# Kernel optimization log

Hardware: AMD Instinct MI355X
Metric: run time of the kernel (lower is better)

The kernel has to match this reference:

```python
import jax, jax.numpy as jnp
import numpy as np
from jax import lax

B, IC, OC, H, W_DIM, K = 8, 64, 64, 256, 512, 3
BLUR_1D = [1.0, 3.0, 3.0, 1.0]
FACTOR = 2
GAIN = 1.0


def _blur_kernel():
    # setup_resample_kernel: outer product of 1D kernel, normalized to sum 1
    k = np.asarray(BLUR_1D, dtype=np.float32)
    k = np.outer(k, k)
    k = k / np.sum(k)
    return k  # [4,4]


def setup_inputs() -> dict:
    key = jax.random.key(0)
    ks = jax.random.split(key, 5)
    x = jax.random.normal(ks[0], (B, IC, H, H), dtype=jnp.float32)
    w = jax.random.normal(ks[1], (B, W_DIM), dtype=jnp.float32)
    # init_std = 1.0 for both weights since lrmul = 1.0
    w_conv = jax.random.normal(ks[2], (K, K, IC, OC), dtype=jnp.float32)
    w_dense = jax.random.normal(ks[3], (W_DIM, IC), dtype=jnp.float32)
    b_mod = jnp.zeros((IC,), dtype=jnp.float32)
    return {"x": x, "w": w, "w_conv": w_conv, "w_dense": w_dense, "b_mod": b_mod}


def reference(x, w, w_conv, w_dense, b_mod):
    k = w_conv.shape[0]
    ic, oc = w_conv.shape[2], w_conv.shape[3]

    # runtime coefs (equalized lr): he_std = gain / sqrt(fan_in), lrmul = 1
    coef_conv = 1.0 / np.sqrt(k * k * ic)
    coef_dense = 1.0 / np.sqrt(w.shape[1])

    # style = Dense(w) + bias (linear act, gain 1) + 1.0   -> [B, IC]
    style = w @ (coef_dense * w_dense) + b_mod + 1.0

    # modulate: [B,k,k,IC,OC]
    wmod = (coef_conv * w_conv)[None] * style[:, None, None, :, None]
    # demodulate over (kh, kw, ic)
    d = lax.rsqrt(jnp.sum(jnp.square(wmod), axis=(1, 2, 3)) + 1e-8)  # [B,OC]
    wmod = wmod * d[:, None, None, None, :]

    # per-sample grouped transposed conv (upsample x2) == lhs-dilated cross-corr
    # with the unflipped modulated weight, padding k-1 on each side.
    w_oihw = jnp.transpose(wmod, (0, 4, 3, 1, 2))  # [B,OC,IC,k,k]

    def up_conv(xb, wb):
        return lax.conv_general_dilated(
            xb[None], wb, window_strides=(1, 1),
            padding=[(k - 1, k - 1), (k - 1, k - 1)],
            lhs_dilation=(FACTOR, FACTOR),
            dimension_numbers=("NCHW", "OIHW", "NCHW"))[0]

    y = jax.vmap(up_conv)(x, w_oihw)  # [B,OC,(H-1)*2+k,(W-1)*2+k] = [B,OC,513,513]

    # upfirdn blur: kernel scaled by gain * factor**2, pad0 = pad1 = 1,
    # true convolution (kernel flipped in reference) applied depthwise.
    kb = jnp.asarray(_blur_kernel() * (GAIN * FACTOR ** 2))  # [4,4]
    fw = kb[::-1, ::-1][None, None]  # [1,1,4,4]
    b_, c_, s1, s2 = y.shape
    y = lax.conv_general_dilated(
        y.reshape(b_ * c_, 1, s1, s2), fw, window_strides=(1, 1),
        padding=[(1, 1), (1, 1)],
        dimension_numbers=("NCHW", "OIHW", "NCHW"))
    # output spatial: s1 + 2 - 4 + 1 = 2H
    return y.reshape(b_, c_, y.shape[2], y.shape[3])
```

## Files before the change

kernel.cpp:

```cpp
#include <hip/hip_runtime.h>

#define NB 8
#define IC 64
#define OC 64
#define HH 256
#define WD 512
#define PP 258

typedef __bf16 bf16x8 __attribute__((ext_vector_type(8)));
typedef float f32x16 __attribute__((ext_vector_type(16)));

__device__ inline void compute_E(const float* __restrict__ w_conv, float stv,
                                 int oc, float E[6][6]) {
  const float coef_conv = 1.0f / 24.0f;
  const float s = stv * coef_conv;
  const int ic = threadIdx.x & 63;

  float wm[3][3];
  float ssq = 0.f;
  #pragma unroll
  for (int kh = 0; kh < 3; ++kh)
    #pragma unroll
    for (int kw = 0; kw < 3; ++kw) {
      float v = w_conv[((kh * 3 + kw) * IC + ic) * OC + oc] * s;
      wm[kh][kw] = v;
      ssq += v * v;
    }
  #pragma unroll
  for (int off = 32; off > 0; off >>= 1) ssq += __shfl_xor(ssq, off);
  const float d = rsqrtf(ssq + 1e-8f);
  #pragma unroll
  for (int kh = 0; kh < 3; ++kh)
    #pragma unroll
    for (int kw = 0; kw < 3; ++kw) wm[kh][kw] *= d;

  const float g[4] = {0.25f, 0.75f, 0.75f, 0.25f};
  #pragma unroll
  for (int a = 0; a < 6; ++a)
    #pragma unroll
    for (int c = 0; c < 6; ++c) {
      float acc = 0.f;
      #pragma unroll
      for (int dh = 0; dh < 3; ++dh) {
        int u = a - dh;
        if (u < 0 || u > 3) continue;
        #pragma unroll
        for (int dw = 0; dw < 3; ++dw) {
          int v = c - dw;
          if (v < 0 || v > 3) continue;
          acc = fmaf(wm[dh][dw], g[u] * g[v], acc);
        }
      }
      E[a][c] = acc;
    }
}

__device__ inline float style_of(const float* __restrict__ w,
                                 const float* __restrict__ w_dense,
                                 const float* __restrict__ b_mod, int b,
                                 int ic) {
  const float coef_dense = 0.044194173824159216f;
  const float* wr = w + b * WD;
  float acc = 0.f;
  for (int k = 0; k < WD; ++k) acc = fmaf(wr[k], w_dense[k * IC + ic], acc);
  return acc * coef_dense + b_mod[ic] + 1.0f;
}

__global__ __launch_bounds__(64) void pwfs_kernel(
    const float* __restrict__ w, const float* __restrict__ w_dense,
    const float* __restrict__ b_mod, const float* __restrict__ w_conv,
    __bf16* __restrict__ PWf) {
  const int oc = blockIdx.x;
  const int b = blockIdx.y;
  const int ic = threadIdx.x;

  float stv = style_of(w, w_dense, b_mod, b, ic);
  float E[6][6];
  compute_E(w_conv, stv, oc, E);

  const int ks = ic >> 4;
  const int h = (ic >> 3) & 1;
  const int e = ic & 7;
  const int lane = (oc & 31) + 32 * h;
  const int ocg = oc >> 5;

  #pragma unroll
  for (int pp = 0; pp < 2; ++pp)
    #pragma unroll
    for (int pq = 0; pq < 2; ++pq) {
      const int ph = pp * 2 + pq;
      #pragma unroll
      for (int j = 0; j < 3; ++j)
        #pragma unroll
        for (int l = 0; l < 3; ++l) {
          const int tap = j * 3 + l;
          float val = E[2 * j + 1 - pp][2 * l + 1 - pq];
          size_t off =
              ((size_t)(((((b * 4 + ph) * 9 + tap) * 2 + ocg) * 4 + ks)) * 64 +
               lane) * 8 + e;
          PWf[off] = (__bf16)val;
        }
    }
}

#define XS 268
__global__ __launch_bounds__(256) void xtp_kernel(const float* __restrict__ x,
                                                  __bf16* __restrict__ xTg) {
  __shared__ unsigned short buf[64 * XS];
  const int tid = threadIdx.x;
  const int m = blockIdx.x;
  const int b = blockIdx.y;

  if (m == 256) {
    uint4 z = make_uint4(0, 0, 0, 0);
    for (int i = tid; i < 8224; i += 256) {
      int pix = i >> 3;
      int sub = i & 7;
      int pr, pc;
      if (pix < 258) {
        pr = 0; pc = pix;
      } else if (pix < 516) {
        pr = 257; pc = pix - 258;
      } else {
        int rem = pix - 516;
        pr = 1 + (rem >> 1);
        pc = (rem & 1) ? 257 : 0;
      }
      *(uint4*)(xTg + ((size_t)(b * PP + pr) * PP + pc) * 64 + sub * 8) = z;
    }
    return;
  }

  const int ln = tid & 63, grp = tid >> 6;
  #pragma unroll
  for (int p = 0; p < 16; ++p) {
    const int ic = p * 4 + grp;
    float4 v = *(const float4*)(x + ((size_t)(b * 64 + ic) * 256 + m) * 256 +
                                ln * 4);
    ushort4 u4;
    u4.x = __builtin_bit_cast(unsigned short, (__bf16)v.x);
    u4.y = __builtin_bit_cast(unsigned short, (__bf16)v.y);
    u4.z = __builtin_bit_cast(unsigned short, (__bf16)v.z);
    u4.w = __builtin_bit_cast(unsigned short, (__bf16)v.w);
    *(ushort4*)&buf[ic * XS + ln * 4] = u4;
  }
  __syncthreads();
  #pragma unroll
  for (int it = 0; it < 8; ++it) {
    int pix = it * 32 + (tid >> 3);
    int g = tid & 7;
    bf16x8 o;
    #pragma unroll
    for (int e = 0; e < 8; ++e)
      o[e] = __builtin_bit_cast(__bf16, buf[(g * 8 + e) * XS + pix]);
    *(bf16x8*)(xTg + ((size_t)(b * PP + m + 1) * PP + (pix + 1)) * 64 +
               g * 8) = o;
  }
}

#define CMT 4
#define XR 6
#define XC 34

#define GLD_LDS(src, dst)                                                \
  __builtin_amdgcn_global_load_lds(                                      \
      (const __attribute__((address_space(1))) void*)(src),              \
      (__attribute__((address_space(3))) void*)(dst), 16, 0, 0)

__device__ __forceinline__ void stage6(const __bf16* __restrict__ xTg, int b,
                                       int m0, int n0, __bf16* xsbuf, int wv,
                                       int lane) {
  if (wv < XR) {
    const int row = wv;
    const size_t srow = (size_t)(b * PP + m0 + row) * PP;
    __bf16* ldsrow = xsbuf + row * (XC * 64);
    #pragma unroll
    for (int q = 0; q < 4; ++q) {
      int pix = q * 8 + (lane >> 3);
      int g = (lane & 7) ^ (pix & 7);
      const __bf16* src = xTg + (srow + (n0 + pix)) * 64 + g * 8;
      GLD_LDS(src, ldsrow + q * 512);
    }
    if (lane < 16) {
      int pix = 32 + (lane >> 3);
      int g = (lane & 7) ^ (pix & 7);
      const __bf16* src = xTg + (srow + (n0 + pix)) * 64 + g * 8;
      GLD_LDS(src, ldsrow + 2048);
    }
  }
}

__global__ __launch_bounds__(512, 2) void conv32a_kernel(
    const __bf16* __restrict__ xTg, const __bf16* __restrict__ PWf,
    float* __restrict__ out) {
  __shared__ __bf16 xs[2][XR * XC * 64];

  const int tid = threadIdx.x;
  const int lane = tid & 63;
  const int wv = tid >> 6;
  const int pq = wv & 1;
  const int pp = (wv >> 1) & 1;
  const int og = wv >> 2;

  const int raw = blockIdx.x;
  const int bid = (raw & 7) * 64 + (raw >> 3);
  const int mtile = bid & 63;
  const int b = bid >> 6;
  const int m0 = mtile * CMT;

  const int ln31 = lane & 31;
  const int lh = lane >> 5;
  const int ph = b * 4 + pp * 2 + pq;
  const bf16x8* Awave =
      (const bf16x8*)PWf + ((size_t)ph * 72 + og * 4) * 64 + lane;

  bf16x8 A[9][4];
  #pragma unroll
  for (int tap = 0; tap < 9; ++tap)
    #pragma unroll
    for (int ks = 0; ks < 4; ++ks) A[tap][ks] = Awave[(tap * 8 + ks) * 64];

  stage6(xTg, b, m0, 0, &xs[0][0], wv, lane);
  asm volatile("s_waitcnt vmcnt(0)" ::: "memory");
  __builtin_amdgcn_s_barrier();

  #pragma unroll 1
  for (int t = 0; t < 8; ++t) {
    const int n0 = t * 32;
    if (t < 7) stage6(xTg, b, m0, n0 + 32, &xs[(t + 1) & 1][0], wv, lane);

    const __bf16* xb = &xs[t & 1][0];

    f32x16 acc[4];
    #pragma unroll
    for (int mw = 0; mw < 4; ++mw)
      #pragma unroll
      for (int e = 0; e < 16; ++e) acc[mw][e] = 0.f;

    #pragma unroll
    for (int ks = 0; ks < 4; ++ks) {
      #pragma unroll
      for (int l = 0; l < 3; ++l) {
        bf16x8 Bf[6];
        const int col_t = ln31 + l;
        const int gneed = ks * 2 + lh;
        #pragma unroll
        for (int r = 0; r < 6; ++r) {
          Bf[r] = *(const bf16x8*)(xb + ((r * XC + col_t) * 8 +
                                         (gneed ^ (col_t & 7))) * 8);
        }
        __builtin_amdgcn_s_setprio(1);
        #pragma unroll
        for (int r = 0; r < 6; ++r) {
          #pragma unroll
          for (int j = 0; j < 3; ++j) {
            const int mw = r - j;
            if (mw >= 0 && mw < 4) {
              acc[mw] = __builtin_amdgcn_mfma_f32_32x32x16_bf16(
                  A[j * 3 + l][ks], Bf[r], acc[mw], 0, 0, 0);
            }
          }
        }
        __builtin_amdgcn_s_setprio(0);
      }
    }

    #pragma unroll
    for (int mw = 0; mw < 4; ++mw) {
      const int p = 2 * (m0 + mw) + pp;
      #pragma unroll
      for (int rr = 0; rr < 16; ++rr) {
        const int oc_loc = (rr & 3) + 8 * (rr >> 2) + 4 * lh;
        const int oc = og * 32 + oc_loc;
        size_t off =
            ((size_t)(b * 64 + oc) * 512 + p) * 512 + 2 * (n0 + ln31) + pq;
        out[off] = acc[mw][rr];
      }
    }

    if (t < 7) {
      asm volatile("s_waitcnt vmcnt(63)" ::: "memory");
      __builtin_amdgcn_s_barrier();
    }
  }
}

__global__ __launch_bounds__(64) void pw_kernel(
    const float* __restrict__ w, const float* __restrict__ w_dense,
    const float* __restrict__ b_mod, const float* __restrict__ w_conv,
    float* __restrict__ PW) {
  const int oc = blockIdx.x;
  const int b = blockIdx.y;
  const int ic = threadIdx.x;
  float stv = style_of(w, w_dense, b_mod, b, ic);
  float E[6][6];
  compute_E(w_conv, stv, oc, E);
  #pragma unroll
  for (int pp = 0; pp < 2; ++pp)
    #pragma unroll
    for (int pq = 0; pq < 2; ++pq)
      #pragma unroll
      for (int j = 0; j < 3; ++j)
        #pragma unroll
        for (int l = 0; l < 3; ++l)
          PW[(((size_t)((b * 4 + pp * 2 + pq) * OC + oc) * IC + ic) * 9) +
             j * 3 + l] = E[2 * j + 1 - pp][2 * l + 1 - pq];
}

#define MT 16
#define NT 64
#define ICC 8
#define XROWS 18
#define XCOLS 66
#define XSTRIDE 68

__global__ __launch_bounds__(256) void conv_kernel(
    const float* __restrict__ x, const float* __restrict__ PW,
    float* __restrict__ out) {
  __shared__ float lds_x[ICC][XROWS][XSTRIDE];
  __shared__ float lds_w[4][ICC][9][4];

  const int tid = threadIdx.x;
  const int tn = tid & 15;
  const int tm = tid >> 4;
  const int bx = blockIdx.x;
  const int ntile = bx & 3;
  const int mtile = bx >> 2;
  const int ocg = blockIdx.y;
  const int b = blockIdx.z;
  const int m0 = mtile * MT;
  const int n0 = ntile * NT;

  float acc[4][4][4];
  #pragma unroll
  for (int o = 0; o < 4; ++o)
    #pragma unroll
    for (int ph = 0; ph < 4; ++ph)
      #pragma unroll
      for (int s = 0; s < 4; ++s) acc[o][ph][s] = 0.f;

  for (int ic0 = 0; ic0 < IC; ic0 += ICC) {
    __syncthreads();
    for (int ici = 0; ici < ICC; ++ici) {
      const float* xsrc = x + (size_t)(b * IC + ic0 + ici) * HH * HH;
      for (int rc = tid; rc < XROWS * XCOLS; rc += 256) {
        int r = rc / XCOLS;
        int c = rc - r * XCOLS;
        int gr = m0 - 1 + r;
        int gc = n0 - 1 + c;
        float v = 0.f;
        if ((unsigned)gr < HH && (unsigned)gc < HH) v = xsrc[gr * HH + gc];
        lds_x[ici][r][c] = v;
      }
    }
    for (int idx = tid; idx < 4 * ICC * 9 * 4; idx += 256) {
      int o = idx / (ICC * 9 * 4);
      int rem = idx - o * (ICC * 9 * 4);
      int ici = rem / 36;
      int r2 = rem - ici * 36;
      int t = r2 >> 2;
      int ph = r2 & 3;
      lds_w[o][ici][t][ph] =
          PW[(((size_t)((b * 4 + ph) * OC + (ocg * 4 + o)) * IC +
               (ic0 + ici)) * 9) + t];
    }
    __syncthreads();
    for (int ici = 0; ici < ICC; ++ici) {
      #pragma unroll
      for (int j = 0; j < 3; ++j) {
        const float* xr = &lds_x[ici][tm + j][tn * 4];
        float4 a4 = *(const float4*)xr;
        float2 a2 = *(const float2*)(xr + 4);
        float xv[6] = {a4.x, a4.y, a4.z, a4.w, a2.x, a2.y};
        #pragma unroll
        for (int l = 0; l < 3; ++l) {
          #pragma unroll
          for (int o = 0; o < 4; ++o) {
            float4 wv = *(const float4*)&lds_w[o][ici][j * 3 + l][0];
            #pragma unroll
            for (int s = 0; s < 4; ++s) {
              acc[o][0][s] = fmaf(wv.x, xv[l + s], acc[o][0][s]);
              acc[o][1][s] = fmaf(wv.y, xv[l + s], acc[o][1][s]);
              acc[o][2][s] = fmaf(wv.z, xv[l + s], acc[o][2][s]);
              acc[o][3][s] = fmaf(wv.w, xv[l + s], acc[o][3][s]);
            }
          }
        }
      }
    }
  }

  #pragma unroll
  for (int o = 0; o < 4; ++o) {
    #pragma unroll
    for (int pp = 0; pp < 2; ++pp) {
      const int p = 2 * (m0 + tm) + pp;
      float* dst = out +
          (((size_t)(b * OC + ocg * 4 + o) * 512 + p) * 512) + 2 * n0 + 8 * tn;
      float4 v0 = make_float4(acc[o][pp * 2 + 0][0], acc[o][pp * 2 + 1][0],
                              acc[o][pp * 2 + 0][1], acc[o][pp * 2 + 1][1]);
      float4 v1 = make_float4(acc[o][pp * 2 + 0][2], acc[o][pp * 2 + 1][2],
                              acc[o][pp * 2 + 0][3], acc[o][pp * 2 + 1][3]);
      *(float4*)dst = v0;
      *(float4*)(dst + 4) = v1;
    }
  }
}

extern "C" void kernel_launch(void* const* d_in, const int* in_sizes, int n_in,
                              void* d_out, int out_size, void* d_ws,
                              size_t ws_size, hipStream_t stream) {
  const float* x = (const float*)d_in[0];
  const float* w = (const float*)d_in[1];
  const float* w_conv = (const float*)d_in[2];
  const float* w_dense = (const float*)d_in[3];
  const float* b_mod = (const float*)d_in[4];
  float* out = (float*)d_out;

  const size_t PWF_BYTES = (size_t)8 * 4 * 9 * 2 * 4 * 64 * 8 * 2;
  const size_t XTG_BYTES = (size_t)8 * PP * PP * 64 * 2;
  const size_t NEED_NEW = PWF_BYTES + XTG_BYTES;

  if (ws_size >= NEED_NEW) {
    __bf16* PWf = (__bf16*)d_ws;
    __bf16* xTg = (__bf16*)((char*)d_ws + PWF_BYTES);
    pwfs_kernel<<<dim3(OC, NB), 64, 0, stream>>>(w, w_dense, b_mod, w_conv,
                                                 PWf);
    xtp_kernel<<<dim3(257, NB), 256, 0, stream>>>(x, xTg);
    conv32a_kernel<<<dim3(512), 512, 0, stream>>>(xTg, PWf, out);
  } else {
    float* PW = (float*)d_ws;
    pw_kernel<<<dim3(OC, NB), 64, 0, stream>>>(w, w_dense, b_mod, w_conv, PW);
    conv_kernel<<<dim3(64, 16, NB), 256, 0, stream>>>(x, PW, out);
  }
}
```

Measured before the change: 256.4 us.

## Merge prep kernels and pair phase outputs via LDS for 8-byte stores

The two preprocessing kernels (weight modulation and x transpose/pad) are merged into one launch, with the weight blocks appended after the transpose blocks, which removes one kernel launch. In the conv epilogue, paired waves with pq=0/1 exchange accumulators through a new LDS buffer so each lane writes two adjacent output columns as one float2 store instead of two strided scalar stores. This adds LDS usage, extra barriers per tile and a changed vmcnt wait, which could hurt occupancy or overlap with the next tile's prefetch.

```diff
diff --git a/kernel.cpp b/kernel.cpp
--- a/kernel.cpp
+++ b/kernel.cpp
@@ -9,6 +9,7 @@
 
 typedef __bf16 bf16x8 __attribute__((ext_vector_type(8)));
 typedef float f32x16 __attribute__((ext_vector_type(16)));
+typedef float f32x2 __attribute__((ext_vector_type(2)));
 
 __device__ inline void compute_E(const float* __restrict__ w_conv, float stv,
                                  int oc, float E[6][6]) {
@@ -66,50 +67,55 @@
   return acc * coef_dense + b_mod[ic] + 1.0f;
 }
 
-__global__ __launch_bounds__(64) void pwfs_kernel(
-    const float* __restrict__ w, const float* __restrict__ w_dense,
-    const float* __restrict__ b_mod, const float* __restrict__ w_conv,
+#define XS 268
+__global__ __launch_bounds__(256) void pre_kernel(
+    const float* __restrict__ x, const float* __restrict__ w,
+    const float* __restrict__ w_dense, const float* __restrict__ b_mod,
+    const float* __restrict__ w_conv, __bf16* __restrict__ xTg,
     __bf16* __restrict__ PWf) {
-  const int oc = blockIdx.x;
-  const int b = blockIdx.y;
-  const int ic = threadIdx.x;
-
-  float stv = style_of(w, w_dense, b_mod, b, ic);
-  float E[6][6];
-  compute_E(w_conv, stv, oc, E);
-
-  const int ks = ic >> 4;
-  const int h = (ic >> 3) & 1;
-  const int e = ic & 7;
-  const int lane = (oc & 31) + 32 * h;
-  const int ocg = oc >> 5;
-
-  #pragma unroll
-  for (int pp = 0; pp < 2; ++pp)
-    #pragma unroll
-    for (int pq = 0; pq < 2; ++pq) {
-      const int ph = pp * 2 + pq;
-      #pragma unroll
-      for (int j = 0; j < 3; ++j)
-        #pragma unroll
-        for (int l = 0; l < 3; ++l) {
-          const int tap = j * 3 + l;
-          float val = E[2 * j + 1 - pp][2 * l + 1 - pq];
-          size_t off =
-              ((size_t)(((((b * 4 + ph) * 9 + tap) * 2 + ocg) * 4 + ks)) * 64 +
-               lane) * 8 + e;
-          PWf[off] = (__bf16)val;
-        }
-    }
-}
-
-#define XS 268
-__global__ __launch_bounds__(256) void xtp_kernel(const float* __restrict__ x,
-                                                  __bf16* __restrict__ xTg) {
   __shared__ unsigned short buf[64 * XS];
   const int tid = threadIdx.x;
-  const int m = blockIdx.x;
-  const int b = blockIdx.y;
+  const int bid = blockIdx.x;
+
+  if (bid >= 2056) {
+    const int bid2 = bid - 2056;
+    const int b = bid2 >> 4;
+    const int ocq = bid2 & 15;
+    const int oc = ocq * 4 + (tid >> 6);
+    const int ic = tid & 63;
+
+    float stv = style_of(w, w_dense, b_mod, b, ic);
+    float E[6][6];
+    compute_E(w_conv, stv, oc, E);
+
+    const int ks = ic >> 4;
+    const int h = (ic >> 3) & 1;
+    const int e = ic & 7;
+    const int lane = (oc & 31) + 32 * h;
+    const int ocg = oc >> 5;
+
+    #pragma unroll
+    for (int pp = 0; pp < 2; ++pp)
+      #pragma unroll
+      for (int pq = 0; pq < 2; ++pq) {
+        const int ph = pp * 2 + pq;
+        #pragma unroll
+        for (int j = 0; j < 3; ++j)
+          #pragma unroll
+          for (int l = 0; l < 3; ++l) {
+            const int tap = j * 3 + l;
+            float val = E[2 * j + 1 - pp][2 * l + 1 - pq];
+            size_t off =
+                ((size_t)(((((b * 4 + ph) * 9 + tap) * 2 + ocg) * 4 + ks)) *
+                     64 + lane) * 8 + e;
+            PWf[off] = (__bf16)val;
+          }
+      }
+    return;
+  }
+
+  const int m = bid % 257;
+  const int b = bid / 257;
 
   if (m == 256) {
     uint4 z = make_uint4(0, 0, 0, 0);
@@ -190,10 +196,11 @@
   }
 }
 
-__global__ __launch_bounds__(512, 2) void conv32a_kernel(
+__global__ __launch_bounds__(512, 2) void conv32e_kernel(
     const __bf16* __restrict__ xTg, const __bf16* __restrict__ PWf,
     float* __restrict__ out) {
   __shared__ __bf16 xs[2][XR * XC * 64];
+  __shared__ float xchg[8][64][18];
 
   const int tid = threadIdx.x;
   const int lane = tid & 63;
@@ -266,21 +273,42 @@
     }
 
     #pragma unroll
-    for (int mw = 0; mw < 4; ++mw) {
-      const int p = 2 * (m0 + mw) + pp;
+    for (int k = 0; k < 2; ++k) {
+      const int mwG = (pq == 0) ? 2 + k : k;
+      const int mwO = (pq == 0) ? k : 2 + k;
+      #pragma unroll
+      for (int q = 0; q < 8; ++q) {
+        f32x2 s;
+        s[0] = acc[mwG][2 * q];
+        s[1] = acc[mwG][2 * q + 1];
+        *(f32x2*)&xchg[wv][lane][2 * q] = s;
+      }
+      __builtin_amdgcn_s_barrier();
+      float po[16];
+      #pragma unroll
+      for (int q = 0; q < 8; ++q) {
+        f32x2 r = *(const f32x2*)&xchg[wv ^ 1][lane][2 * q];
+        po[2 * q] = r[0];
+        po[2 * q + 1] = r[1];
+      }
+      const int p = 2 * (m0 + mwO) + pp;
       #pragma unroll
       for (int rr = 0; rr < 16; ++rr) {
         const int oc_loc = (rr & 3) + 8 * (rr >> 2) + 4 * lh;
         const int oc = og * 32 + oc_loc;
         size_t off =
-            ((size_t)(b * 64 + oc) * 512 + p) * 512 + 2 * (n0 + ln31) + pq;
-        out[off] = acc[mw][rr];
-      }
-    }
-
-    if (t < 7) {
-      asm volatile("s_waitcnt vmcnt(63)" ::: "memory");
-      __builtin_amdgcn_s_barrier();
+            ((size_t)(b * 64 + oc) * 512 + p) * 512 + 2 * (n0 + ln31);
+        f32x2 v2;
+        v2[0] = (pq == 0) ? acc[mwO][rr] : po[rr];
+        v2[1] = (pq == 0) ? po[rr] : acc[mwO][rr];
+        *(f32x2*)(out + off) = v2;
+      }
+      if (k == 0) {
+        __builtin_amdgcn_s_barrier();
+      } else if (t < 7) {
+        asm volatile("s_waitcnt vmcnt(32)" ::: "memory");
+        __builtin_amdgcn_s_barrier();
+      }
     }
   }
 }
@@ -424,10 +452,9 @@
   if (ws_size >= NEED_NEW) {
     __bf16* PWf = (__bf16*)d_ws;
     __bf16* xTg = (__bf16*)((char*)d_ws + PWF_BYTES);
-    pwfs_kernel<<<dim3(OC, NB), 64, 0, stream>>>(w, w_dense, b_mod, w_conv,
-                                                 PWf);
-    xtp_kernel<<<dim3(257, NB), 256, 0, stream>>>(x, xTg);
-    conv32a_kernel<<<dim3(512), 512, 0, stream>>>(xTg, PWf, out);
+    pre_kernel<<<dim3(2056 + 128), 256, 0, stream>>>(x, w, w_dense, b_mod,
+                                                     w_conv, xTg, PWf);
+    conv32e_kernel<<<dim3(512), 512, 0, stream>>>(xTg, PWf, out);
   } else {
     float* PW = (float*)d_ws;
     pw_kernel<<<dim3(OC, NB), 64, 0, stream>>>(w, w_dense, b_mod, w_conv, PW);
```

After: 257.5 us. Within noise of the previous version (+0.4%).
